# Kernel tuning notes

Measured on AMD Instinct MI355X. Metric: run time of the kernel, lower is better.

## Reference

```python
import jax, jax.numpy as jnp
import numpy as np

P = 1048576   # total sampled points
N = 8192      # rays
E = 8         # experts
H = 128       # expert hidden dim
TOP_K = 2
INTERVAL = 0.5      # stepsize * voxel_size_ratio
ACT_SHIFT = -4.0    # models[-1].act_shift
THRESH = 1e-4       # fast_color_thres (ndc=False)


def raw2alpha(d):
    # Raw2Alpha: alpha = 1 - exp(-softplus(density + act_shift) * interval)
    return 1.0 - jnp.exp(-jax.nn.softplus(d + ACT_SHIFT) * INTERVAL)


def alphas2weights(alpha, ray_id, n_rays):
    # Sequential per-ray transmittance: w_j = alpha_j * prod_{k<j in ray}(1 - alpha_k)
    la = jnp.log1p(-jnp.clip(alpha, 0.0, 1.0 - 1e-6))      # [P], <= 0
    cum = jnp.cumsum(la)
    excl = cum - la                                          # exclusive cumsum, nonincreasing
    # offset per ray = excl at first point of the (sorted) segment == segment max
    offset = jax.ops.segment_max(excl, ray_id, num_segments=n_rays)
    T = jnp.exp(excl - offset[ray_id])                       # transmittance before each point
    weights = alpha * T
    alphainv_last = jnp.exp(jax.ops.segment_sum(la, ray_id, num_segments=n_rays))
    return weights, alphainv_last


def setup_inputs() -> dict:
    key = jax.random.key(0)
    ks = jax.random.split(key, 12)
    s = 0.3  # weight scale keeping activations in a sane range
    return {
        "ray_pts": jax.random.uniform(ks[0], (P, 3), dtype=jnp.float32),
        "viewdirs": jax.random.normal(ks[1], (N, 3), dtype=jnp.float32),
        "bg": jnp.ones((3,), dtype=jnp.float32),
        "Wd1": jax.random.normal(ks[2], (3, H), dtype=jnp.float32) * s,
        "bd1": jnp.zeros((H,), dtype=jnp.float32),
        "Wd2": jax.random.normal(ks[3], (H, 1), dtype=jnp.float32) * s,
        "Wg": jax.random.normal(ks[4], (6, E), dtype=jnp.float32) * s,
        "We1": jax.random.normal(ks[5], (E, 6, H), dtype=jnp.float32) * s,
        "be1": jnp.zeros((E, H), dtype=jnp.float32),
        "Wrgb": jax.random.normal(ks[6], (E, H, 3), dtype=jnp.float32) * s,
        "Walpha": jax.random.normal(ks[7], (E, H, 1), dtype=jnp.float32) * s,
        "ray_id": jnp.sort(jax.random.randint(ks[8], (P,), 0, N)).astype(jnp.int32),
    }


def reference(ray_pts, viewdirs, bg, Wd1, bd1, Wd2, Wg, We1, be1, Wrgb, Walpha, ray_id):
    # --- density grid query + activation ---
    hd = jax.nn.relu(ray_pts @ Wd1 + bd1)                    # [P,H]
    density = (hd @ Wd2)[:, 0]                               # [P]
    alpha0 = raw2alpha(density)
    # filter low density (zeroing alpha == dropping the point from the cumprod)
    alpha0 = jnp.where(alpha0 > THRESH, alpha0, 0.0)
    w0, _ = alphas2weights(alpha0, ray_id, N)
    # filter low transmittance (w0 <= THRESH also covers alpha0 == 0)
    keep = w0 > THRESH                                        # [P] bool

    # --- gate: softmax over experts, top-k, renormalize ---
    x = jnp.concatenate([ray_pts, viewdirs[ray_id]], axis=-1)  # [P,6]
    probs = jax.nn.softmax(x @ Wg, axis=-1)                    # [P,E]
    vals, idx = jax.lax.top_k(probs, TOP_K)                    # [P,K]
    vals = vals / jnp.sum(vals, axis=-1, keepdims=True)        # top_k > 1
    g = jnp.sum(vals[..., None] * jax.nn.one_hot(idx, E, dtype=vals.dtype), axis=1)  # [P,E]
    g = g * keep[:, None].astype(g.dtype)

    # --- per-expert radiance / alpha, mixed by gate weights ---
    rgb = jnp.zeros((ray_pts.shape[0], 3), dtype=ray_pts.dtype)
    alpha_mix = jnp.zeros((ray_pts.shape[0],), dtype=ray_pts.dtype)
    for e in range(E):  # fixed small expert count
        h = jax.nn.relu(x @ We1[e] + be1[e])                   # [P,H]
        rgb_e = jax.nn.sigmoid(h @ Wrgb[e])                    # [P,3]
        a_e = raw2alpha((h @ Walpha[e])[:, 0])                 # [P]
        rgb = rgb + g[:, e:e + 1] * rgb_e
        alpha_mix = alpha_mix + g[:, e] * a_e

    # --- composite: Alphas2Weights + segment_coo sum + background ---
    w, alphainv_last = alphas2weights(alpha_mix, ray_id, N)
    rgb_marched = jax.ops.segment_sum(w[:, None] * rgb, ray_id, num_segments=N)
    rgb_marched = rgb_marched + alphainv_last[:, None] * bg
    return rgb_marched
```

## Files before the change

kernel.cpp:

```cpp
#include <hip/hip_runtime.h>

#define PTOT   1048576
#define NRAYS  8192
#define THRESH 1e-4f

typedef float F2 __attribute__((ext_vector_type(2)));

__device__ __forceinline__ F2 f2splat(float s){ F2 r; r.x = s; r.y = s; return r; }
__device__ __forceinline__ F2 f2fma(F2 a, float b, F2 c){
    return __builtin_elementwise_fma(a, f2splat(b), c);
}
__device__ __forceinline__ float raw2alpha_f(float d){
    return 1.0f - rsqrtf(1.0f + __expf(d - 4.0f));
}

__global__ __launch_bounds__(256) void k_point(
    const float* __restrict__ pts, const float* __restrict__ vdirs,
    const int* __restrict__ ray_id,
    const float* __restrict__ Wd1, const float* __restrict__ bd1,
    const float* __restrict__ Wd2, const float* __restrict__ Wg,
    float* __restrict__ alpha0, float* __restrict__ g0a, int* __restrict__ eea,
    float4* __restrict__ vd, int* __restrict__ ray_off)
{
    __shared__ float4 WD4[128];
    __shared__ float  WD2s[128];
    __shared__ float  WGs[8][6];
    int t = threadIdx.x;
    if (t < 128){
        WD4[t] = make_float4(Wd1[t], Wd1[128+t], Wd1[256+t], bd1[t]);
        WD2s[t] = Wd2[t];
    }
    if (t < 48) WGs[t & 7][t >> 3] = Wg[t];
    __syncthreads();

    int base = blockIdx.x * 2048 + t;
    F2 px[4], py[4], pz[4], vx[4], vy[4], vz[4], dens[4];
    int rid0[4], rid1[4];
    #pragma unroll
    for (int q=0;q<4;q++){
        int p0 = base + (2*q)*256, p1 = p0 + 256;
        px[q] = (F2){pts[3*p0],   pts[3*p1]};
        py[q] = (F2){pts[3*p0+1], pts[3*p1+1]};
        pz[q] = (F2){pts[3*p0+2], pts[3*p1+2]};
        int r0 = ray_id[p0], r1 = ray_id[p1];
        rid0[q] = r0; rid1[q] = r1;
        vx[q] = (F2){vdirs[3*r0],   vdirs[3*r1]};
        vy[q] = (F2){vdirs[3*r0+1], vdirs[3*r1+1]};
        vz[q] = (F2){vdirs[3*r0+2], vdirs[3*r1+2]};
        dens[q] = f2splat(0.f);
    }
    #pragma unroll
    for (int q=0;q<4;q++){
        int p0 = base + (2*q)*256, p1 = p0 + 256;
        vd[p0] = make_float4(vx[q].x, vy[q].x, vz[q].x, 0.f);
        vd[p1] = make_float4(vx[q].y, vy[q].y, vz[q].y, 0.f);
        int prev0 = (p0 == 0) ? -1 : ray_id[p0-1];
        if (prev0 != rid0[q]) for (int r=prev0+1; r<=rid0[q]; ++r) ray_off[r] = p0;
        int prev1 = ray_id[p1-1];
        if (prev1 != rid1[q]) for (int r=prev1+1; r<=rid1[q]; ++r) ray_off[r] = p1;
        if (p1 == PTOT-1) for (int r=rid1[q]+1; r<=NRAYS; ++r) ray_off[r] = PTOT;
    }
    #pragma unroll 2
    for (int i=0;i<128;i++){
        float4 w = WD4[i]; float w2 = WD2s[i];
        #pragma unroll
        for (int q=0;q<4;q++){
            F2 h = f2fma(px[q], w.x, f2fma(py[q], w.y, f2fma(pz[q], w.z, f2splat(w.w))));
            h = __builtin_elementwise_max(h, f2splat(0.f));
            dens[q] = f2fma(h, w2, dens[q]);
        }
    }
    #pragma unroll
    for (int q=0;q<4;q++){
        float a0 = raw2alpha_f(dens[q].x);
        float a1 = raw2alpha_f(dens[q].y);
        alpha0[base + (2*q)*256]   = (a0 > THRESH) ? a0 : 0.f;
        alpha0[base + (2*q+1)*256] = (a1 > THRESH) ? a1 : 0.f;
    }
    float m0[8], m1[8]; int i0[8], i1[8];
    #pragma unroll
    for (int j=0;j<8;j++){ m0[j]=-3.0e38f; m1[j]=-3.0e38f; i0[j]=0; i1[j]=0; }
    for (int e=0;e<8;e++){
        float w0=WGs[e][0],w1=WGs[e][1],w2=WGs[e][2],w3=WGs[e][3],w4=WGs[e][4],w5=WGs[e][5];
        #pragma unroll
        for (int q=0;q<4;q++){
            F2 l = f2fma(px[q],w0, f2fma(py[q],w1, f2fma(pz[q],w2,
                   f2fma(vx[q],w3, f2fma(vy[q],w4,
                   __builtin_elementwise_fma(vz[q], f2splat(w5), f2splat(0.f)))))));
            int j0 = 2*q, j1 = 2*q+1;
            float lx = l.x, ly = l.y;
            if (lx > m0[j0]){ m1[j0]=m0[j0]; i1[j0]=i0[j0]; m0[j0]=lx; i0[j0]=e; }
            else if (lx > m1[j0]){ m1[j0]=lx; i1[j0]=e; }
            if (ly > m0[j1]){ m1[j1]=m0[j1]; i1[j1]=i0[j1]; m0[j1]=ly; i0[j1]=e; }
            else if (ly > m1[j1]){ m1[j1]=ly; i1[j1]=e; }
        }
    }
    #pragma unroll
    for (int j=0;j<8;j++){
        float g0 = __fdividef(1.0f, 1.0f + __expf(m1[j]-m0[j]));
        g0a[base + j*256] = g0;
        eea[base + j*256] = i0[j] | (i1[j] << 8);
    }
}

__global__ __launch_bounds__(256) void k_scan0(const float* __restrict__ alpha0,
                                               const int* __restrict__ eea,
                                               const int* __restrict__ ray_off,
                                               unsigned char* __restrict__ keep,
                                               int* __restrict__ cntA)
{
    __shared__ int wcs[4][8];
    int t = threadIdx.x, lane = t & 63, w = t >> 6;
    int wid = blockIdx.x*4 + w;
    int c[8];
    #pragma unroll
    for (int e=0;e<8;e++) c[e]=0;
    int s = ray_off[wid], e = ray_off[wid+1];
    float carry = 1.f;
    for (int ch = s; ch < e; ch += 64){
        int p = ch + lane;
        bool in = p < e;
        float a = in ? alpha0[p] : 0.f;
        int  ee = in ? eea[p] : 0;
        float incl = 1.f - a;
        #pragma unroll
        for (int d=1; d<64; d<<=1){ float tt = __shfl_up(incl, d); if (lane >= d) incl *= tt; }
        float excl = __shfl_up(incl, 1); if (lane == 0) excl = 1.f;
        float w0 = a * carry * excl;
        int k = (in && w0 > THRESH) ? 1 : 0;
        if (in) keep[p] = (unsigned char)k;
        int e0 = ee & 255, e1 = (ee >> 8) & 255;
        #pragma unroll
        for (int x=0;x<8;x++){
            unsigned long long m0 = __ballot(k && e0==x);
            unsigned long long m1 = __ballot(k && e1==x);
            c[x] += __popcll(m0) + __popcll(m1);
        }
        carry *= __shfl(incl, 63);
    }
    if (lane == 0){
        #pragma unroll
        for (int x=0;x<8;x++) wcs[w][x] = c[x];
    }
    __syncthreads();
    if (t < 8){
        int sum = wcs[0][t]+wcs[1][t]+wcs[2][t]+wcs[3][t];
        if (sum) atomicAdd(&cntA[t], sum);
    }
}

__global__ __launch_bounds__(256) void k_fill(const unsigned char* __restrict__ keep,
                                              const float* __restrict__ g0a,
                                              const int* __restrict__ eea,
                                              const int* __restrict__ cntA,
                                              int* __restrict__ curA,
                                              int2* __restrict__ ent)
{
    __shared__ int wc[4][8];
    __shared__ int wb[4][8];
    __shared__ int sOff[8];
    int t = threadIdx.x, lane = t & 63, w = t >> 6;
    unsigned long long lt = (1ull << lane) - 1ull;
    int base = blockIdx.x * 2048;

    int c[8];
    #pragma unroll
    for (int e=0;e<8;e++) c[e]=0;
    for (int j=0;j<8;j++){
        int p = base + (j*4 + w)*64 + lane;
        int k = keep[p];
        int ee = eea[p];
        int e0 = ee & 255, e1 = (ee >> 8) & 255;
        #pragma unroll
        for (int e=0;e<8;e++){
            unsigned long long m0 = __ballot(k && e0==e);
            unsigned long long m1 = __ballot(k && e1==e);
            c[e] += __popcll(m0) + __popcll(m1);
        }
    }
    if (lane == 0){
        #pragma unroll
        for (int e=0;e<8;e++) wc[w][e] = c[e];
    }
    if (t == 0){
        int acc = 0;
        for (int e=0;e<8;e++){ sOff[e] = acc; acc += cntA[e]; }
    }
    __syncthreads();
    if (t < 8){
        int tot = wc[0][t]+wc[1][t]+wc[2][t]+wc[3][t];
        int b = sOff[t] + (tot ? atomicAdd(&curA[t], tot) : 0);
        wb[0][t] = b; b += wc[0][t];
        wb[1][t] = b; b += wc[1][t];
        wb[2][t] = b; b += wc[2][t];
        wb[3][t] = b;
    }
    __syncthreads();

    int cur[8];
    #pragma unroll
    for (int e=0;e<8;e++) cur[e] = wb[w][e];
    for (int j=0;j<8;j++){
        int p = base + (j*4 + w)*64 + lane;
        int k = keep[p];
        float g0 = g0a[p];
        int ee = eea[p];
        int e0 = ee & 255, e1 = (ee >> 8) & 255;
        #pragma unroll
        for (int e=0;e<8;e++){
            unsigned long long m0 = __ballot(k && e0==e);
            unsigned long long m1 = __ballot(k && e1==e);
            if (k && e0==e)
                ent[cur[e] + __popcll(m0 & lt)] = make_int2(p, __float_as_int(g0));
            if (k && e1==e)
                ent[cur[e] + __popcll(m0) + __popcll(m1 & lt)] =
                    make_int2(p | (1 << 30), __float_as_int(1.0f - g0));
            cur[e] += __popcll(m0) + __popcll(m1);
        }
    }
}

__global__ __launch_bounds__(256) void k_expert(
    const int2* __restrict__ ent, const int* __restrict__ cntA,
    const float* __restrict__ pts, const float4* __restrict__ vd,
    const float* __restrict__ We1, const float* __restrict__ be1,
    const float* __restrict__ Wrgb, const float* __restrict__ Walpha,
    float4* __restrict__ res)
{
    int k = blockIdx.x;
    int e = -1, s0 = 0, n = 0, base = 0;
    int acc = 0, sacc = 0;
    #pragma unroll
    for (int i=0;i<8;i++){
        int c  = cntA[i];
        int ch = (c + 2047) >> 11;
        if (e < 0 && k < acc + ch){ e = i; s0 = sacc; n = c; base = (k - acc) << 11; }
        acc  += ch;
        sacc += c;
    }
    if (e < 0) return;

    __shared__ float4 WA[128];
    __shared__ float4 WB[128];
    __shared__ float4 WC[128];
    int t = threadIdx.x;
    if (t < 128){
        const float* w = We1 + e*768;
        WA[t] = make_float4(w[t], w[128+t], w[256+t], w[384+t]);
        WB[t] = make_float4(w[512+t], w[640+t], be1[e*128+t], Walpha[e*128+t]);
        const float* wr = Wrgb + e*384 + 3*t;
        WC[t] = make_float4(wr[0], wr[1], wr[2], 0.f);
    }
    __syncthreads();
    const int2* eb = ent + s0;

    F2 x0[4],x1[4],x2[4],x3[4],x4[4],x5[4];
    F2 ar[4],ag[4],ab[4],aa[4];
    #pragma unroll
    for (int pr=0;pr<4;pr++){
        int idx0 = base + t + (2*pr)*256, idx1 = idx0 + 256;
        int2 r0 = (idx0 < n) ? eb[idx0] : make_int2(0,0);
        int2 r1 = (idx1 < n) ? eb[idx1] : make_int2(0,0);
        int p0 = r0.x & 0x0FFFFFFF, p1 = r1.x & 0x0FFFFFFF;
        x0[pr] = (F2){pts[3*p0],   pts[3*p1]};
        x1[pr] = (F2){pts[3*p0+1], pts[3*p1+1]};
        x2[pr] = (F2){pts[3*p0+2], pts[3*p1+2]};
        float4 v0 = vd[p0], v1 = vd[p1];
        x3[pr] = (F2){v0.x, v1.x};
        x4[pr] = (F2){v0.y, v1.y};
        x5[pr] = (F2){v0.z, v1.z};
        ar[pr] = f2splat(0.f); ag[pr] = f2splat(0.f);
        ab[pr] = f2splat(0.f); aa[pr] = f2splat(0.f);
    }
    #pragma unroll 2
    for (int i=0;i<128;i++){
        float4 wa = WA[i], wb = WB[i], wc = WC[i];
        #pragma unroll
        for (int pr=0;pr<4;pr++){
            F2 h = f2fma(x0[pr],wa.x, f2fma(x1[pr],wa.y, f2fma(x2[pr],wa.z,
                   f2fma(x3[pr],wa.w, f2fma(x4[pr],wb.x, f2fma(x5[pr],wb.y,
                   f2splat(wb.z)))))));
            h = __builtin_elementwise_max(h, f2splat(0.f));
            ar[pr] = f2fma(h, wc.x, ar[pr]);
            ag[pr] = f2fma(h, wc.y, ag[pr]);
            ab[pr] = f2fma(h, wc.z, ab[pr]);
            aa[pr] = f2fma(h, wb.w, aa[pr]);
        }
    }
    #pragma unroll
    for (int pr=0;pr<4;pr++){
        #pragma unroll
        for (int sel=0; sel<2; sel++){
            int idx = base + t + (2*pr+sel)*256;
            if (idx < n){
                int2 rec = eb[idx];
                float vr = sel ? ar[pr].y : ar[pr].x;
                float vg = sel ? ag[pr].y : ag[pr].x;
                float vb = sel ? ab[pr].y : ab[pr].x;
                float va = sel ? aa[pr].y : aa[pr].x;
                float sr = __fdividef(1.0f, 1.0f + __expf(-vr));
                float sg = __fdividef(1.0f, 1.0f + __expf(-vg));
                float sb = __fdividef(1.0f, 1.0f + __expf(-vb));
                float a  = raw2alpha_f(va);
                float g  = __int_as_float(rec.y);
                int pp   = rec.x & 0x0FFFFFFF;
                int slot = ((unsigned)rec.x) >> 30;
                res[2*(size_t)pp + slot] = make_float4(g*sr, g*sg, g*sb, g*a);
            }
        }
    }
}

__global__ __launch_bounds__(256) void k_scan1(const float4* __restrict__ res,
                                               const unsigned char* __restrict__ keep,
                                               const int* __restrict__ ray_off,
                                               const float* __restrict__ bg,
                                               float* __restrict__ out)
{
    int wid  = (blockIdx.x*blockDim.x + threadIdx.x) >> 6;
    int lane = threadIdx.x & 63;
    if (wid >= NRAYS) return;
    int s = ray_off[wid], e = ray_off[wid+1];
    float carry = 1.f;
    float accx = 0.f, accy = 0.f, accz = 0.f;
    for (int c = s; c < e; c += 64){
        int p = c + lane;
        float4 v = make_float4(0.f,0.f,0.f,0.f);
        if (p < e && keep[p]){
            float4 v0 = res[2*(size_t)p];
            float4 v1 = res[2*(size_t)p + 1];
            v = make_float4(v0.x+v1.x, v0.y+v1.y, v0.z+v1.z, v0.w+v1.w);
        }
        float a = v.w;
        float incl = 1.f - a;
        #pragma unroll
        for (int d=1; d<64; d<<=1){ float tt = __shfl_up(incl, d); if (lane >= d) incl *= tt; }
        float excl = __shfl_up(incl, 1); if (lane == 0) excl = 1.f;
        float w = a * carry * excl;
        accx = fmaf(w, v.x, accx);
        accy = fmaf(w, v.y, accy);
        accz = fmaf(w, v.z, accz);
        carry *= __shfl(incl, 63);
    }
    #pragma unroll
    for (int d=32; d; d>>=1){
        accx += __shfl_xor(accx, d);
        accy += __shfl_xor(accy, d);
        accz += __shfl_xor(accz, d);
    }
    if (lane == 0){
        out[3*wid+0] = accx + carry*bg[0];
        out[3*wid+1] = accy + carry*bg[1];
        out[3*wid+2] = accz + carry*bg[2];
    }
}

extern "C" void kernel_launch(void* const* d_in, const int* in_sizes, int n_in,
                              void* d_out, int out_size, void* d_ws, size_t ws_size,
                              hipStream_t stream)
{
    const float* pts    = (const float*)d_in[0];
    const float* vdirs  = (const float*)d_in[1];
    const float* bg     = (const float*)d_in[2];
    const float* Wd1    = (const float*)d_in[3];
    const float* bd1    = (const float*)d_in[4];
    const float* Wd2    = (const float*)d_in[5];
    const float* Wg     = (const float*)d_in[6];
    const float* We1    = (const float*)d_in[7];
    const float* be1    = (const float*)d_in[8];
    const float* Wrgb   = (const float*)d_in[9];
    const float* Walpha = (const float*)d_in[10];
    const int*   ray_id = (const int*)d_in[11];
    float* out = (float*)d_out;

    char* ws = (char*)d_ws;
    size_t off = 0;
    float* alpha0        = (float*)(ws + off); off += (size_t)PTOT*4;
    float* g0a           = (float*)(ws + off); off += (size_t)PTOT*4;
    int*   eea           = (int*)  (ws + off); off += (size_t)PTOT*4;
    unsigned char* keep  = (unsigned char*)(ws + off); off += (size_t)PTOT;
    int*   ray_off       = (int*)  (ws + off); off += 33024;
    int*   cntA          = (int*)  (ws + off); off += 256;
    int*   curA          = (int*)  (ws + off); off += 256;
    off = (off + 255) & ~(size_t)255;
    float4* vd           = (float4*)(ws + off); off += (size_t)PTOT*16;
    int2*  ent           = (int2*) (ws + off); off += (size_t)2*PTOT*8;
    float4* res          = (float4*)(ws + off); off += ((size_t)2*PTOT+2)*16;

    hipMemsetAsync(cntA, 0, 512, stream);

    k_point <<<PTOT/2048, 256, 0, stream>>>(pts, vdirs, ray_id, Wd1, bd1, Wd2, Wg,
                                            alpha0, g0a, eea, vd, ray_off);
    k_scan0 <<<NRAYS/4, 256, 0, stream>>>(alpha0, eea, ray_off, keep, cntA);
    k_fill  <<<PTOT/2048, 256, 0, stream>>>(keep, g0a, eea, cntA, curA, ent);
    k_expert<<<1032, 256, 0, stream>>>(ent, cntA, pts, vd,
                                       We1, be1, Wrgb, Walpha, res);
    k_scan1 <<<NRAYS*64/256, 256, 0, stream>>>(res, keep, ray_off, bg, out);
}
```

Baseline: 243.5 us.

## Fuse scan and fill kernels with per-expert fixed-capacity buckets, drop vd buffer

Merges the per-ray transmittance scan with the expert bucket fill into one kernel that appends into fixed-capacity per-expert regions. This removes the separate fill pass and its re-read of keep/eea/g0a, along with the second atomic counter. It also drops the materialised per-point viewdir buffer: the expert kernel gathers vdirs through ray_id instead, trading a 16 MB write for an extra indirection. k_point halves its points per block for more blocks, and the workspace aliases res over alpha0/g0a/eea. The per-ray order of bucket entries changes, so expert work becomes less spatially ordered.

```diff
diff --git a/kernel.cpp b/kernel.cpp
--- a/kernel.cpp
+++ b/kernel.cpp
@@ -3,6 +3,7 @@
 #define PTOT   1048576
 #define NRAYS  8192
 #define THRESH 1e-4f
+#define ECAP   PTOT
 
 typedef float F2 __attribute__((ext_vector_type(2)));
 
@@ -20,7 +21,7 @@
     const float* __restrict__ Wd1, const float* __restrict__ bd1,
     const float* __restrict__ Wd2, const float* __restrict__ Wg,
     float* __restrict__ alpha0, float* __restrict__ g0a, int* __restrict__ eea,
-    float4* __restrict__ vd, int* __restrict__ ray_off)
+    int* __restrict__ ray_off)
 {
     __shared__ float4 WD4[128];
     __shared__ float  WD2s[128];
@@ -33,11 +34,11 @@
     if (t < 48) WGs[t & 7][t >> 3] = Wg[t];
     __syncthreads();
 
-    int base = blockIdx.x * 2048 + t;
-    F2 px[4], py[4], pz[4], vx[4], vy[4], vz[4], dens[4];
-    int rid0[4], rid1[4];
-    #pragma unroll
-    for (int q=0;q<4;q++){
+    int base = blockIdx.x * 1024 + t;
+    F2 px[2], py[2], pz[2], vx[2], vy[2], vz[2], dens[2];
+    int rid0[2], rid1[2];
+    #pragma unroll
+    for (int q=0;q<2;q++){
         int p0 = base + (2*q)*256, p1 = p0 + 256;
         px[q] = (F2){pts[3*p0],   pts[3*p1]};
         py[q] = (F2){pts[3*p0+1], pts[3*p1+1]};
@@ -50,10 +51,8 @@
         dens[q] = f2splat(0.f);
     }
     #pragma unroll
-    for (int q=0;q<4;q++){
+    for (int q=0;q<2;q++){
         int p0 = base + (2*q)*256, p1 = p0 + 256;
-        vd[p0] = make_float4(vx[q].x, vy[q].x, vz[q].x, 0.f);
-        vd[p1] = make_float4(vx[q].y, vy[q].y, vz[q].y, 0.f);
         int prev0 = (p0 == 0) ? -1 : ray_id[p0-1];
         if (prev0 != rid0[q]) for (int r=prev0+1; r<=rid0[q]; ++r) ray_off[r] = p0;
         int prev1 = ray_id[p1-1];
@@ -64,26 +63,26 @@
     for (int i=0;i<128;i++){
         float4 w = WD4[i]; float w2 = WD2s[i];
         #pragma unroll
-        for (int q=0;q<4;q++){
+        for (int q=0;q<2;q++){
             F2 h = f2fma(px[q], w.x, f2fma(py[q], w.y, f2fma(pz[q], w.z, f2splat(w.w))));
             h = __builtin_elementwise_max(h, f2splat(0.f));
             dens[q] = f2fma(h, w2, dens[q]);
         }
     }
     #pragma unroll
-    for (int q=0;q<4;q++){
+    for (int q=0;q<2;q++){
         float a0 = raw2alpha_f(dens[q].x);
         float a1 = raw2alpha_f(dens[q].y);
         alpha0[base + (2*q)*256]   = (a0 > THRESH) ? a0 : 0.f;
         alpha0[base + (2*q+1)*256] = (a1 > THRESH) ? a1 : 0.f;
     }
-    float m0[8], m1[8]; int i0[8], i1[8];
-    #pragma unroll
-    for (int j=0;j<8;j++){ m0[j]=-3.0e38f; m1[j]=-3.0e38f; i0[j]=0; i1[j]=0; }
+    float m0[4], m1[4]; int i0[4], i1[4];
+    #pragma unroll
+    for (int j=0;j<4;j++){ m0[j]=-3.0e38f; m1[j]=-3.0e38f; i0[j]=0; i1[j]=0; }
     for (int e=0;e<8;e++){
         float w0=WGs[e][0],w1=WGs[e][1],w2=WGs[e][2],w3=WGs[e][3],w4=WGs[e][4],w5=WGs[e][5];
         #pragma unroll
-        for (int q=0;q<4;q++){
+        for (int q=0;q<2;q++){
             F2 l = f2fma(px[q],w0, f2fma(py[q],w1, f2fma(pz[q],w2,
                    f2fma(vx[q],w3, f2fma(vy[q],w4,
                    __builtin_elementwise_fma(vz[q], f2splat(w5), f2splat(0.f)))))));
@@ -96,26 +95,29 @@
         }
     }
     #pragma unroll
-    for (int j=0;j<8;j++){
+    for (int j=0;j<4;j++){
         float g0 = __fdividef(1.0f, 1.0f + __expf(m1[j]-m0[j]));
         g0a[base + j*256] = g0;
         eea[base + j*256] = i0[j] | (i1[j] << 8);
     }
 }
 
-__global__ __launch_bounds__(256) void k_scan0(const float* __restrict__ alpha0,
-                                               const int* __restrict__ eea,
-                                               const int* __restrict__ ray_off,
-                                               unsigned char* __restrict__ keep,
-                                               int* __restrict__ cntA)
+__global__ __launch_bounds__(256) void k_scanfill(
+    const float* __restrict__ alpha0, const int* __restrict__ eea,
+    const float* __restrict__ g0a, const int* __restrict__ ray_off,
+    unsigned char* __restrict__ keep, int* __restrict__ cntA,
+    int2* __restrict__ ent)
 {
     __shared__ int wcs[4][8];
+    __shared__ int wb[4][8];
     int t = threadIdx.x, lane = t & 63, w = t >> 6;
+    unsigned long long lt = (1ull << lane) - 1ull;
     int wid = blockIdx.x*4 + w;
+    int s = ray_off[wid], e = ray_off[wid+1];
+
     int c[8];
     #pragma unroll
-    for (int e=0;e<8;e++) c[e]=0;
-    int s = ray_off[wid], e = ray_off[wid+1];
+    for (int x=0;x<8;x++) c[x]=0;
     float carry = 1.f;
     for (int ch = s; ch < e; ch += 64){
         int p = ch + lane;
@@ -144,99 +146,56 @@
     }
     __syncthreads();
     if (t < 8){
-        int sum = wcs[0][t]+wcs[1][t]+wcs[2][t]+wcs[3][t];
-        if (sum) atomicAdd(&cntA[t], sum);
-    }
-}
-
-__global__ __launch_bounds__(256) void k_fill(const unsigned char* __restrict__ keep,
-                                              const float* __restrict__ g0a,
-                                              const int* __restrict__ eea,
-                                              const int* __restrict__ cntA,
-                                              int* __restrict__ curA,
-                                              int2* __restrict__ ent)
-{
-    __shared__ int wc[4][8];
-    __shared__ int wb[4][8];
-    __shared__ int sOff[8];
-    int t = threadIdx.x, lane = t & 63, w = t >> 6;
-    unsigned long long lt = (1ull << lane) - 1ull;
-    int base = blockIdx.x * 2048;
-
-    int c[8];
-    #pragma unroll
-    for (int e=0;e<8;e++) c[e]=0;
-    for (int j=0;j<8;j++){
-        int p = base + (j*4 + w)*64 + lane;
-        int k = keep[p];
-        int ee = eea[p];
+        int tot = wcs[0][t]+wcs[1][t]+wcs[2][t]+wcs[3][t];
+        int b = tot ? atomicAdd(&cntA[t], tot) : 0;
+        wb[0][t] = b; b += wcs[0][t];
+        wb[1][t] = b; b += wcs[1][t];
+        wb[2][t] = b; b += wcs[2][t];
+        wb[3][t] = b;
+    }
+    __syncthreads();
+    int cur[8];
+    #pragma unroll
+    for (int x=0;x<8;x++) cur[x] = x*ECAP + wb[w][x];
+
+    for (int ch = s; ch < e; ch += 64){
+        int p = ch + lane;
+        bool in = p < e;
+        int  k  = in ? keep[p] : 0;
+        int  ee = in ? eea[p] : 0;
+        float g0 = in ? g0a[p] : 0.f;
         int e0 = ee & 255, e1 = (ee >> 8) & 255;
         #pragma unroll
-        for (int e=0;e<8;e++){
-            unsigned long long m0 = __ballot(k && e0==e);
-            unsigned long long m1 = __ballot(k && e1==e);
-            c[e] += __popcll(m0) + __popcll(m1);
-        }
-    }
-    if (lane == 0){
-        #pragma unroll
-        for (int e=0;e<8;e++) wc[w][e] = c[e];
-    }
-    if (t == 0){
-        int acc = 0;
-        for (int e=0;e<8;e++){ sOff[e] = acc; acc += cntA[e]; }
-    }
-    __syncthreads();
-    if (t < 8){
-        int tot = wc[0][t]+wc[1][t]+wc[2][t]+wc[3][t];
-        int b = sOff[t] + (tot ? atomicAdd(&curA[t], tot) : 0);
-        wb[0][t] = b; b += wc[0][t];
-        wb[1][t] = b; b += wc[1][t];
-        wb[2][t] = b; b += wc[2][t];
-        wb[3][t] = b;
-    }
-    __syncthreads();
-
-    int cur[8];
-    #pragma unroll
-    for (int e=0;e<8;e++) cur[e] = wb[w][e];
-    for (int j=0;j<8;j++){
-        int p = base + (j*4 + w)*64 + lane;
-        int k = keep[p];
-        float g0 = g0a[p];
-        int ee = eea[p];
-        int e0 = ee & 255, e1 = (ee >> 8) & 255;
-        #pragma unroll
-        for (int e=0;e<8;e++){
-            unsigned long long m0 = __ballot(k && e0==e);
-            unsigned long long m1 = __ballot(k && e1==e);
-            if (k && e0==e)
-                ent[cur[e] + __popcll(m0 & lt)] = make_int2(p, __float_as_int(g0));
-            if (k && e1==e)
-                ent[cur[e] + __popcll(m0) + __popcll(m1 & lt)] =
+        for (int x=0;x<8;x++){
+            unsigned long long m0 = __ballot(k && e0==x);
+            unsigned long long m1 = __ballot(k && e1==x);
+            if (k && e0==x)
+                ent[cur[x] + __popcll(m0 & lt)] = make_int2(p, __float_as_int(g0));
+            if (k && e1==x)
+                ent[cur[x] + __popcll(m0) + __popcll(m1 & lt)] =
                     make_int2(p | (1 << 30), __float_as_int(1.0f - g0));
-            cur[e] += __popcll(m0) + __popcll(m1);
+            cur[x] += __popcll(m0) + __popcll(m1);
         }
     }
 }
 
 __global__ __launch_bounds__(256) void k_expert(
     const int2* __restrict__ ent, const int* __restrict__ cntA,
-    const float* __restrict__ pts, const float4* __restrict__ vd,
+    const float* __restrict__ pts, const int* __restrict__ ray_id,
+    const float* __restrict__ vdirs,
     const float* __restrict__ We1, const float* __restrict__ be1,
     const float* __restrict__ Wrgb, const float* __restrict__ Walpha,
     float4* __restrict__ res)
 {
     int k = blockIdx.x;
-    int e = -1, s0 = 0, n = 0, base = 0;
-    int acc = 0, sacc = 0;
+    int e = -1, n = 0, base = 0;
+    int acc = 0;
     #pragma unroll
     for (int i=0;i<8;i++){
         int c  = cntA[i];
         int ch = (c + 2047) >> 11;
-        if (e < 0 && k < acc + ch){ e = i; s0 = sacc; n = c; base = (k - acc) << 11; }
-        acc  += ch;
-        sacc += c;
+        if (e < 0 && k < acc + ch){ e = i; n = c; base = (k - acc) << 11; }
+        acc += ch;
     }
     if (e < 0) return;
 
@@ -252,7 +211,7 @@
         WC[t] = make_float4(wr[0], wr[1], wr[2], 0.f);
     }
     __syncthreads();
-    const int2* eb = ent + s0;
+    const int2* eb = ent + (size_t)e * ECAP;
 
     F2 x0[4],x1[4],x2[4],x3[4],x4[4],x5[4];
     F2 ar[4],ag[4],ab[4],aa[4];
@@ -262,13 +221,13 @@
         int2 r0 = (idx0 < n) ? eb[idx0] : make_int2(0,0);
         int2 r1 = (idx1 < n) ? eb[idx1] : make_int2(0,0);
         int p0 = r0.x & 0x0FFFFFFF, p1 = r1.x & 0x0FFFFFFF;
+        int ra = ray_id[p0], rb = ray_id[p1];
         x0[pr] = (F2){pts[3*p0],   pts[3*p1]};
         x1[pr] = (F2){pts[3*p0+1], pts[3*p1+1]};
         x2[pr] = (F2){pts[3*p0+2], pts[3*p1+2]};
-        float4 v0 = vd[p0], v1 = vd[p1];
-        x3[pr] = (F2){v0.x, v1.x};
-        x4[pr] = (F2){v0.y, v1.y};
-        x5[pr] = (F2){v0.z, v1.z};
+        x3[pr] = (F2){vdirs[3*ra],   vdirs[3*rb]};
+        x4[pr] = (F2){vdirs[3*ra+1], vdirs[3*rb+1]};
+        x5[pr] = (F2){vdirs[3*ra+2], vdirs[3*rb+2]};
         ar[pr] = f2splat(0.f); ag[pr] = f2splat(0.f);
         ab[pr] = f2splat(0.f); aa[pr] = f2splat(0.f);
     }
@@ -375,25 +334,25 @@
 
     char* ws = (char*)d_ws;
     size_t off = 0;
-    float* alpha0        = (float*)(ws + off); off += (size_t)PTOT*4;
-    float* g0a           = (float*)(ws + off); off += (size_t)PTOT*4;
-    int*   eea           = (int*)  (ws + off); off += (size_t)PTOT*4;
     unsigned char* keep  = (unsigned char*)(ws + off); off += (size_t)PTOT;
     int*   ray_off       = (int*)  (ws + off); off += 33024;
     int*   cntA          = (int*)  (ws + off); off += 256;
-    int*   curA          = (int*)  (ws + off); off += 256;
     off = (off + 255) & ~(size_t)255;
-    float4* vd           = (float4*)(ws + off); off += (size_t)PTOT*16;
-    int2*  ent           = (int2*) (ws + off); off += (size_t)2*PTOT*8;
-    float4* res          = (float4*)(ws + off); off += ((size_t)2*PTOT+2)*16;
-
-    hipMemsetAsync(cntA, 0, 512, stream);
-
-    k_point <<<PTOT/2048, 256, 0, stream>>>(pts, vdirs, ray_id, Wd1, bd1, Wd2, Wg,
-                                            alpha0, g0a, eea, vd, ray_off);
-    k_scan0 <<<NRAYS/4, 256, 0, stream>>>(alpha0, eea, ray_off, keep, cntA);
-    k_fill  <<<PTOT/2048, 256, 0, stream>>>(keep, g0a, eea, cntA, curA, ent);
-    k_expert<<<1032, 256, 0, stream>>>(ent, cntA, pts, vd,
-                                       We1, be1, Wrgb, Walpha, res);
-    k_scan1 <<<NRAYS*64/256, 256, 0, stream>>>(res, keep, ray_off, bg, out);
-}
+    size_t offA = off;
+    float* alpha0        = (float*)(ws + offA);
+    float* g0a           = (float*)(ws + offA + (size_t)PTOT*4);
+    int*   eea           = (int*)  (ws + offA + (size_t)PTOT*8);
+    float4* res          = (float4*)(ws + offA);
+    size_t resBytes      = ((size_t)2*PTOT + 2) * 16;
+    size_t offE          = (offA + resBytes + 255) & ~(size_t)255;
+    int2*  ent           = (int2*) (ws + offE);
+
+    hipMemsetAsync(cntA, 0, 256, stream);
+
+    k_point   <<<PTOT/1024, 256, 0, stream>>>(pts, vdirs, ray_id, Wd1, bd1, Wd2, Wg,
+                                              alpha0, g0a, eea, ray_off);
+    k_scanfill<<<NRAYS/4, 256, 0, stream>>>(alpha0, eea, g0a, ray_off, keep, cntA, ent);
+    k_expert  <<<1032, 256, 0, stream>>>(ent, cntA, pts, ray_id, vdirs,
+                                         We1, be1, Wrgb, Walpha, res);
+    k_scan1   <<<NRAYS*64/256, 256, 0, stream>>>(res, keep, ray_off, bg, out);
+}
```

New measurement: 223.2 us. 1.09x faster.
